# Optimization experiments

Measured on AMD Instinct MI355X. Metric: run time of the kernel, lower is better.

## Reference

```python
import jax, jax.numpy as jnp
import numpy as np

N_S, N_T, E, B = 100000, 100000, 3200000, 16
F_XS, F_XT, F_E, F_U = 10, 5, 10, 10


def setup_inputs() -> dict:
    key = jax.random.key(0)
    ks = jax.random.split(key, 8)
    x_s = jax.random.normal(ks[0], (N_S, F_XS), dtype=jnp.float32)
    x_t = jax.random.normal(ks[1], (N_T, F_XT), dtype=jnp.float32)
    edge_index = jax.random.randint(ks[2], (2, E), 0, N_S, dtype=jnp.int64)
    edge_attr = jax.random.normal(ks[3], (E, F_E), dtype=jnp.float32)
    u = jax.random.normal(ks[4], (B, F_U), dtype=jnp.float32)
    batch_e = jax.random.randint(ks[5], (E,), 0, B, dtype=jnp.int64)
    F_in = F_XS + F_XT + F_E + F_U  # 35
    W1 = jax.random.normal(ks[6], (F_in, F_E), dtype=jnp.float32) / np.sqrt(F_in)
    b1 = jnp.zeros((F_E,), dtype=jnp.float32)
    W2 = jax.random.normal(ks[7], (F_E, F_E), dtype=jnp.float32) / np.sqrt(F_E)
    b2 = jnp.zeros((F_E,), dtype=jnp.float32)
    return {"x_s": x_s, "x_t": x_t, "edge_index": edge_index,
            "edge_attr": edge_attr, "u": u, "batch_e": batch_e,
            "W1": W1, "b1": b1, "W2": W2, "b2": b2}


def reference(x_s, x_t, edge_index, edge_attr, u, batch_e, W1, b1, W2, b2):
    src, tgt = edge_index[0], edge_index[1]
    # [E, 35] concat of gathered per-node, per-edge, per-graph features
    out = jnp.concatenate([x_s[src], x_t[tgt], edge_attr, u[batch_e]], axis=1)
    h = out @ W1 + b1
    h = jnp.where(h >= 0, h, 0.1 * h)  # LeakyReLU(0.1)
    return h @ W2 + b2
```

## Files before the change

kernel.cpp:

```cpp
#include <hip/hip_runtime.h>
#include <hip/hip_fp16.h>

typedef float f2v __attribute__((ext_vector_type(2)));
typedef float f4v __attribute__((ext_vector_type(4)));

struct __attribute__((packed, aligned(8))) Row24 {
    uint2 ab;
    uint2 cd;
    uint  e;
    uint  pad;
};

__device__ __forceinline__ float2 h2f2(uint v) {
    __half2 h = *(__half2*)&v;
    return __half22float2(h);
}

__global__ __launch_bounds__(256) void prep_as(const float* __restrict__ xs,
                                               const float* __restrict__ W1,
                                               Row24* __restrict__ As, int N) {
    const int n = blockIdx.x * 256 + threadIdx.x;
    if (n >= N) return;
    float f[10];
    const float2* p = (const float2*)(xs + (size_t)n * 10);
    #pragma unroll
    for (int i = 0; i < 5; ++i) { float2 v = p[i]; f[2 * i] = v.x; f[2 * i + 1] = v.y; }
    float a[10];
    #pragma unroll
    for (int j = 0; j < 10; ++j) a[j] = 0.f;
    #pragma unroll
    for (int k = 0; k < 10; ++k) {
        const float fk = f[k];
        #pragma unroll
        for (int j = 0; j < 10; ++j) a[j] += fk * W1[k * 10 + j];
    }
    uint q[5];
    #pragma unroll
    for (int i = 0; i < 5; ++i) {
        __half2 h = __floats2half2_rn(a[2 * i], a[2 * i + 1]);
        q[i] = *(uint*)&h;
    }
    Row24 r;
    r.ab = make_uint2(q[0], q[1]);
    r.cd = make_uint2(q[2], q[3]);
    r.e  = q[4];
    r.pad = 0;
    As[n] = r;
}

__global__ __launch_bounds__(256) void prep_xt(const float* __restrict__ xt,
                                               uint4* __restrict__ Xt, int N) {
    const int n = blockIdx.x * 256 + threadIdx.x;
    if (n >= N) return;
    float f[5];
    #pragma unroll
    for (int i = 0; i < 5; ++i) f[i] = xt[(size_t)n * 5 + i];
    __half2 h01 = __floats2half2_rn(f[0], f[1]);
    __half2 h23 = __floats2half2_rn(f[2], f[3]);
    __half2 h4_ = __floats2half2_rn(f[4], 0.f);
    uint4 r;
    r.x = *(uint*)&h01;
    r.y = *(uint*)&h23;
    r.z = *(uint*)&h4_;
    r.w = 0;
    Xt[n] = r;
}

__device__ __forceinline__ void mlp_edge(const float* __restrict__ g,
                                         Row24 ra, uint4 rt, int ib,
                                         const float* __restrict__ sUp,
                                         const float* __restrict__ W1,
                                         const float* __restrict__ W2,
                                         const float* __restrict__ b2,
                                         float* __restrict__ o)
{
    float h[10];
    {
        uint qa[5] = { ra.ab.x, ra.ab.y, ra.cd.x, ra.cd.y, ra.e };
        #pragma unroll
        for (int i = 0; i < 5; ++i) {
            float2 a2 = h2f2(qa[i]);
            h[2 * i]     = a2.x + sUp[ib * 12 + 2 * i];
            h[2 * i + 1] = a2.y + sUp[ib * 12 + 2 * i + 1];
        }
    }
    {
        float2 t01 = h2f2(rt.x), t23 = h2f2(rt.y), t4_ = h2f2(rt.z);
        const float tv[5] = { t01.x, t01.y, t23.x, t23.y, t4_.x };
        #pragma unroll
        for (int k = 0; k < 5; ++k) {
            const float fk = tv[k];
            #pragma unroll
            for (int j = 0; j < 10; ++j) h[j] += fk * W1[(10 + k) * 10 + j];
        }
    }
    #pragma unroll
    for (int k = 0; k < 10; ++k) {
        const float gk = g[k];
        #pragma unroll
        for (int j = 0; j < 10; ++j) h[j] += gk * W1[(15 + k) * 10 + j];
    }
    #pragma unroll
    for (int j = 0; j < 10; ++j) h[j] = (h[j] >= 0.f) ? h[j] : 0.1f * h[j];

    #pragma unroll
    for (int j = 0; j < 10; ++j) o[j] = b2[j];
    #pragma unroll
    for (int k = 0; k < 10; ++k) {
        const float hk = h[k];
        #pragma unroll
        for (int j = 0; j < 10; ++j) o[j] += hk * W2[k * 10 + j];
    }
}

__global__ __launch_bounds__(256) void edge_mlp_stage(
    const Row24* __restrict__ As,
    const uint4* __restrict__ Xt,
    const int* __restrict__ src,
    const int* __restrict__ tgt,
    const float* __restrict__ ea,
    const float* __restrict__ u,
    const int* __restrict__ be,
    const float* __restrict__ W1,
    const float* __restrict__ b1,
    const float* __restrict__ W2,
    const float* __restrict__ b2,
    float* __restrict__ out, int E)
{
    __shared__ float sUp[16 * 12];
    __shared__ float stage[2560];

    const int t = threadIdx.x;
    if (t < 160) {
        const int b = t / 10, j = t % 10;
        float acc = b1[j];
        #pragma unroll
        for (int k = 0; k < 10; ++k) acc += u[b * 10 + k] * W1[(25 + k) * 10 + j];
        sUp[b * 12 + j] = acc;
    }

    const int  base_e = blockIdx.x * 256;
    const long long base_f = (long long)base_e * 10;
    const bool full = (base_e + 256) <= E;

    if (full) {
        const f4v* pe = (const f4v*)(ea + base_f);
        #pragma unroll
        for (int r = 0; r < 3; ++r) {
            int i = t + r * 256;
            if (i < 640) ((f4v*)stage)[i] = __builtin_nontemporal_load(pe + i);
        }
    } else {
        const long long totalf = (long long)E * 10;
        for (int i = t; i < 2560; i += 256)
            if (base_f + i < totalf) stage[i] = ea[base_f + i];
    }
    __syncthreads();

    const int e = base_e + t;
    float o[10];
    bool valid = e < E;
    if (valid) {
        const int is = __builtin_nontemporal_load(src + e);
        const int it = __builtin_nontemporal_load(tgt + e);
        const int ib = __builtin_nontemporal_load(be + e);

        Row24 ra = As[is];
        uint4 rt = Xt[it];

        float g[10];
        const f2v* pg = (const f2v*)&stage[t * 10];
        #pragma unroll
        for (int i = 0; i < 5; ++i) { f2v v = pg[i]; g[2 * i] = v[0]; g[2 * i + 1] = v[1]; }

        mlp_edge(g, ra, rt, ib, sUp, W1, W2, b2, o);
    }

    if (full) {
        __syncthreads();
        #pragma unroll
        for (int i = 0; i < 5; ++i) {
            f2v v; v[0] = o[2 * i]; v[1] = o[2 * i + 1];
            *(f2v*)&stage[t * 10 + 2 * i] = v;
        }
        __syncthreads();
        f4v* po = (f4v*)(out + base_f);
        #pragma unroll
        for (int r = 0; r < 3; ++r) {
            int i = t + r * 256;
            if (i < 640) po[i] = ((const f4v*)stage)[i];
        }
    } else if (valid) {
        float2* po = (float2*)(out + (size_t)e * 10);
        #pragma unroll
        for (int i = 0; i < 5; ++i) { float2 v; v.x = o[2 * i]; v.y = o[2 * i + 1]; po[i] = v; }
    }
}

__global__ __launch_bounds__(256) void edge_mlp_raw(
    const float* __restrict__ xs, const float* __restrict__ xt,
    const int* __restrict__ src, const int* __restrict__ tgt,
    const float* __restrict__ ea, const float* __restrict__ u,
    const int* __restrict__ be,
    const float* __restrict__ W1, const float* __restrict__ b1,
    const float* __restrict__ W2, const float* __restrict__ b2,
    float* __restrict__ out, int E)
{
    __shared__ float sUp[16 * 12];
    const int t = threadIdx.x;
    if (t < 160) {
        const int b = t / 10, j = t % 10;
        float acc = b1[j];
        #pragma unroll
        for (int k = 0; k < 10; ++k) acc += u[b * 10 + k] * W1[(25 + k) * 10 + j];
        sUp[b * 12 + j] = acc;
    }
    __syncthreads();
    const int e = blockIdx.x * 256 + t;
    if (e >= E) return;
    const int is = src[e], it = tgt[e], ib = be[e];
    float f[25];
    const float* ps = xs + (size_t)is * 10;
    #pragma unroll
    for (int i = 0; i < 5; ++i) {
        float2 v = *(const float2*)(ps + 2 * i);
        f[2 * i] = v.x; f[2 * i + 1] = v.y;
    }
    const float* pt = xt + (size_t)it * 5;
    #pragma unroll
    for (int i = 0; i < 5; ++i) f[10 + i] = pt[i];
    const float2* pe = (const float2*)(ea + (size_t)e * 10);
    #pragma unroll
    for (int i = 0; i < 5; ++i) { float2 v = pe[i]; f[15 + 2 * i] = v.x; f[16 + 2 * i] = v.y; }
    float h[10];
    #pragma unroll
    for (int j = 0; j < 10; ++j) h[j] = sUp[ib * 12 + j];
    #pragma unroll
    for (int k = 0; k < 25; ++k) {
        const float fk = f[k];
        #pragma unroll
        for (int j = 0; j < 10; ++j) h[j] += fk * W1[k * 10 + j];
    }
    #pragma unroll
    for (int j = 0; j < 10; ++j) h[j] = (h[j] >= 0.f) ? h[j] : 0.1f * h[j];
    float o[10];
    #pragma unroll
    for (int j = 0; j < 10; ++j) o[j] = b2[j];
    #pragma unroll
    for (int k = 0; k < 10; ++k) {
        const float hk = h[k];
        #pragma unroll
        for (int j = 0; j < 10; ++j) o[j] += hk * W2[k * 10 + j];
    }
    float2* po = (float2*)(out + (size_t)e * 10);
    #pragma unroll
    for (int i = 0; i < 5; ++i) { float2 v; v.x = o[2 * i]; v.y = o[2 * i + 1]; po[i] = v; }
}

extern "C" void kernel_launch(void* const* d_in, const int* in_sizes, int n_in,
                              void* d_out, int out_size, void* d_ws, size_t ws_size,
                              hipStream_t stream) {
    const float* x_s      = (const float*)d_in[0];
    const float* x_t      = (const float*)d_in[1];
    const int*   ei       = (const int*)d_in[2];
    const float* edge_att = (const float*)d_in[3];
    const float* u        = (const float*)d_in[4];
    const int*   batch_e  = (const int*)d_in[5];
    const float* W1       = (const float*)d_in[6];
    const float* b1       = (const float*)d_in[7];
    const float* W2       = (const float*)d_in[8];
    const float* b2       = (const float*)d_in[9];
    float* out = (float*)d_out;

    const int E   = in_sizes[5];
    const int N_S = in_sizes[0] / 10;
    const int N_T = in_sizes[1] / 5;
    const int blocks = (E + 255) / 256;

    const size_t need = (size_t)N_S * sizeof(Row24) + (size_t)N_T * sizeof(uint4);
    if (ws_size >= need) {
        Row24* As = (Row24*)d_ws;
        uint4* Xt = (uint4*)((char*)d_ws + (size_t)N_S * sizeof(Row24));
        prep_as<<<(N_S + 255) / 256, 256, 0, stream>>>(x_s, W1, As, N_S);
        prep_xt<<<(N_T + 255) / 256, 256, 0, stream>>>(x_t, Xt, N_T);
        edge_mlp_stage<<<blocks, 256, 0, stream>>>(
            As, Xt, ei, ei + E, edge_att, u, batch_e,
            W1, b1, W2, b2, out, E);
    } else {
        edge_mlp_raw<<<blocks, 256, 0, stream>>>(
            x_s, x_t, ei, ei + E, edge_att, u, batch_e,
            W1, b1, W2, b2, out, E);
    }
}
```

Before: 104.7 us.

## Persistent double-buffered edge kernel with async global-to-LDS prefetch

Turns the one-tile-per-block edge kernel into a persistent grid-stride kernel capped at 1792 blocks. Each block prefetches the next tile's edge attributes straight into a second LDS buffer with global_load_lds, and loads its indices, while it computes the current tile. The aim is to hide global load latency and spread the per-block setup (the u·W1 precompute) across many tiles. The cost is twice the LDS per block, which can lower occupancy, plus extra barriers and a fixed grid size.

```diff
diff --git a/kernel.cpp b/kernel.cpp
--- a/kernel.cpp
+++ b/kernel.cpp
@@ -3,6 +3,9 @@
 
 typedef float f2v __attribute__((ext_vector_type(2)));
 typedef float f4v __attribute__((ext_vector_type(4)));
+
+#define LDS_AS __attribute__((address_space(3)))
+#define GLB_AS __attribute__((address_space(1)))
 
 struct __attribute__((packed, aligned(8))) Row24 {
     uint2 ab;
@@ -113,7 +116,7 @@
     }
 }
 
-__global__ __launch_bounds__(256) void edge_mlp_stage(
+__global__ __launch_bounds__(256) void edge_mlp_dbuf(
     const Row24* __restrict__ As,
     const uint4* __restrict__ Xt,
     const int* __restrict__ src,
@@ -125,10 +128,10 @@
     const float* __restrict__ b1,
     const float* __restrict__ W2,
     const float* __restrict__ b2,
-    float* __restrict__ out, int E)
+    float* __restrict__ out, int E, int ntiles)
 {
     __shared__ float sUp[16 * 12];
-    __shared__ float stage[2560];
+    __shared__ __align__(16) float stage[2][2560];
 
     const int t = threadIdx.x;
     if (t < 160) {
@@ -139,61 +142,106 @@
         sUp[b * 12 + j] = acc;
     }
 
-    const int  base_e = blockIdx.x * 256;
-    const long long base_f = (long long)base_e * 10;
-    const bool full = (base_e + 256) <= E;
-
-    if (full) {
-        const f4v* pe = (const f4v*)(ea + base_f);
-        #pragma unroll
-        for (int r = 0; r < 3; ++r) {
-            int i = t + r * 256;
-            if (i < 640) ((f4v*)stage)[i] = __builtin_nontemporal_load(pe + i);
-        }
-    } else {
-        const long long totalf = (long long)E * 10;
-        for (int i = t; i < 2560; i += 256)
-            if (base_f + i < totalf) stage[i] = ea[base_f + i];
-    }
+    int tile = blockIdx.x;
+    const int tstride = gridDim.x;
+    if (tile >= ntiles) return;
+
+    const int wave_base4 = (t & ~63) * 4;
+
+    auto stage_tile = [&](int tl, int buf) {
+        const int base_e = tl * 256;
+        if (base_e + 256 <= E) {
+            const float* gsrc = ea + (size_t)base_e * 10;
+            {
+                const float* g0 = gsrc + (size_t)t * 4;
+                float* l0 = &stage[buf][wave_base4];
+                __builtin_amdgcn_global_load_lds((const GLB_AS uint*)g0, (LDS_AS uint*)l0, 16, 0, 0);
+            }
+            {
+                const float* g1 = gsrc + (size_t)(256 + t) * 4;
+                float* l1 = &stage[buf][1024 + wave_base4];
+                __builtin_amdgcn_global_load_lds((const GLB_AS uint*)g1, (LDS_AS uint*)l1, 16, 0, 0);
+            }
+            if (t < 128) {
+                const float* g2 = gsrc + (size_t)(512 + t) * 4;
+                float* l2 = &stage[buf][2048 + wave_base4];
+                __builtin_amdgcn_global_load_lds((const GLB_AS uint*)g2, (LDS_AS uint*)l2, 16, 0, 0);
+            }
+        } else {
+            const long long base_f = (long long)base_e * 10;
+            const long long totalf = (long long)E * 10;
+            for (int i = t; i < 2560; i += 256)
+                if (base_f + i < totalf) stage[buf][i] = ea[base_f + i];
+        }
+    };
+    auto load_idx = [&](int tl, int& is, int& it, int& ib) {
+        long long e = (long long)tl * 256 + t;
+        long long c = (e < E) ? e : (long long)(E - 1);
+        is = __builtin_nontemporal_load(src + c);
+        it = __builtin_nontemporal_load(tgt + c);
+        ib = __builtin_nontemporal_load(be + c);
+    };
+
+    int cur = 0;
+    stage_tile(tile, 0);
+    int is0, it0, ib0;
+    load_idx(tile, is0, it0, ib0);
     __syncthreads();
 
-    const int e = base_e + t;
-    float o[10];
-    bool valid = e < E;
-    if (valid) {
-        const int is = __builtin_nontemporal_load(src + e);
-        const int it = __builtin_nontemporal_load(tgt + e);
-        const int ib = __builtin_nontemporal_load(be + e);
-
-        Row24 ra = As[is];
-        uint4 rt = Xt[it];
-
-        float g[10];
-        const f2v* pg = (const f2v*)&stage[t * 10];
-        #pragma unroll
-        for (int i = 0; i < 5; ++i) { f2v v = pg[i]; g[2 * i] = v[0]; g[2 * i + 1] = v[1]; }
-
-        mlp_edge(g, ra, rt, ib, sUp, W1, W2, b2, o);
-    }
-
-    if (full) {
-        __syncthreads();
-        #pragma unroll
-        for (int i = 0; i < 5; ++i) {
-            f2v v; v[0] = o[2 * i]; v[1] = o[2 * i + 1];
-            *(f2v*)&stage[t * 10 + 2 * i] = v;
-        }
-        __syncthreads();
-        f4v* po = (f4v*)(out + base_f);
-        #pragma unroll
-        for (int r = 0; r < 3; ++r) {
-            int i = t + r * 256;
-            if (i < 640) po[i] = ((const f4v*)stage)[i];
-        }
-    } else if (valid) {
-        float2* po = (float2*)(out + (size_t)e * 10);
-        #pragma unroll
-        for (int i = 0; i < 5; ++i) { float2 v; v.x = o[2 * i]; v.y = o[2 * i + 1]; po[i] = v; }
+    for (;;) {
+        const int ntile = tile + tstride;
+        const bool have_next = ntile < ntiles;
+
+        int is1, it1, ib1;
+        if (have_next) {
+            stage_tile(ntile, cur ^ 1);
+            load_idx(ntile, is1, it1, ib1);
+        }
+
+        const int base_e = tile * 256;
+        const int e = base_e + t;
+        const bool full = (base_e + 256) <= E;
+        const bool valid = e < E;
+        float o[10];
+        if (valid) {
+            Row24 ra = As[is0];
+            uint4 rt = Xt[it0];
+            float g[10];
+            const f2v* pg = (const f2v*)&stage[cur][t * 10];
+            #pragma unroll
+            for (int i = 0; i < 5; ++i) { f2v v = pg[i]; g[2 * i] = v[0]; g[2 * i + 1] = v[1]; }
+            mlp_edge(g, ra, rt, ib0, sUp, W1, W2, b2, o);
+        }
+
+        if (full) {
+            #pragma unroll
+            for (int i = 0; i < 5; ++i) {
+                f2v v; v[0] = o[2 * i]; v[1] = o[2 * i + 1];
+                *(f2v*)&stage[cur][t * 10 + 2 * i] = v;
+            }
+            __syncthreads();
+            const f4v* sp = (const f4v*)stage[cur];
+            f4v* po = (f4v*)(out + (size_t)base_e * 10);
+            po[t] = sp[t];
+            po[t + 256] = sp[t + 256];
+            if (t < 128) po[t + 512] = sp[t + 512];
+        } else {
+            __syncthreads();
+            if (valid) {
+                float2* po = (float2*)(out + (size_t)e * 10);
+                #pragma unroll
+                for (int i = 0; i < 5; ++i) { float2 v; v.x = o[2 * i]; v.y = o[2 * i + 1]; po[i] = v; }
+            }
+        }
+
+        if (!have_next) break;
+
+        __builtin_amdgcn_sched_barrier(0);
+        __builtin_amdgcn_s_barrier();
+        __builtin_amdgcn_sched_barrier(0);
+
+        tile = ntile; cur ^= 1;
+        is0 = is1; it0 = it1; ib0 = ib1;
     }
 }
 
@@ -275,7 +323,6 @@
     const int E   = in_sizes[5];
     const int N_S = in_sizes[0] / 10;
     const int N_T = in_sizes[1] / 5;
-    const int blocks = (E + 255) / 256;
 
     const size_t need = (size_t)N_S * sizeof(Row24) + (size_t)N_T * sizeof(uint4);
     if (ws_size >= need) {
@@ -283,10 +330,13 @@
         uint4* Xt = (uint4*)((char*)d_ws + (size_t)N_S * sizeof(Row24));
         prep_as<<<(N_S + 255) / 256, 256, 0, stream>>>(x_s, W1, As, N_S);
         prep_xt<<<(N_T + 255) / 256, 256, 0, stream>>>(x_t, Xt, N_T);
-        edge_mlp_stage<<<blocks, 256, 0, stream>>>(
+        const int ntiles = (E + 255) / 256;
+        const int blocks = (ntiles < 1792) ? ntiles : 1792;
+        edge_mlp_dbuf<<<blocks, 256, 0, stream>>>(
             As, Xt, ei, ei + E, edge_att, u, batch_e,
-            W1, b1, W2, b2, out, E);
+            W1, b1, W2, b2, out, E, ntiles);
     } else {
+        const int blocks = (E + 255) / 256;
         edge_mlp_raw<<<blocks, 256, 0, stream>>>(
             x_s, x_t, ei, ei + E, edge_att, u, batch_e,
             W1, b1, W2, b2, out, E);
```

After: 102.4 us. -2.1%, faster.
